# Optimization experiments

Hardware: AMD Instinct MI355X
Metric: run time of the kernel (lower is better)

Reference implementation:

```python
import jax, jax.numpy as jnp
import numpy as np

B, S, H = 4, 2048, 576
NH, NKV, HD = 9, 3, 64
GROUPS = NH // NKV
ROPE_THETA = 100000.0
MAX_POS = 8192


def _rope_tables():
    inv_freq = 1.0 / (ROPE_THETA ** (jnp.arange(0, HD, 2, dtype=jnp.float32) / HD))
    t = jnp.arange(MAX_POS, dtype=jnp.float32)
    freqs = jnp.outer(t, inv_freq)              # [MAX_POS, HD//2]
    emb = jnp.concatenate([freqs, freqs], axis=-1)  # [MAX_POS, HD]
    return jnp.cos(emb), jnp.sin(emb)


def _rotate_half(x):
    x1, x2 = x[..., : HD // 2], x[..., HD // 2 :]
    return jnp.concatenate([-x2, x1], axis=-1)


def setup_inputs() -> dict:
    key = jax.random.key(0)
    k1, k2, k3, k4, k5 = jax.random.split(key, 5)
    hidden_states = jax.random.normal(k1, (B, S, H), dtype=jnp.float32)
    # causal additive mask [B,1,S,S]: 0 where allowed, large negative above diagonal
    causal = jnp.triu(jnp.ones((S, S), dtype=bool), k=1)
    attention_mask = jnp.where(causal, jnp.float32(-1e9), jnp.float32(0.0))[None, None]
    attention_mask = jnp.broadcast_to(attention_mask, (B, 1, S, S))
    position_ids = jnp.broadcast_to(jnp.arange(S, dtype=jnp.int32)[None, :], (B, S))
    scale = 1.0 / np.sqrt(H)
    Wq = jax.random.normal(k2, (NH * HD, H), dtype=jnp.float32) * scale
    Wk = jax.random.normal(k3, (NKV * HD, H), dtype=jnp.float32) * scale
    Wv = jax.random.normal(k4, (NKV * HD, H), dtype=jnp.float32) * scale
    Wo = jax.random.normal(k5, (H, NH * HD), dtype=jnp.float32) * scale
    return {"hidden_states": hidden_states, "attention_mask": attention_mask,
            "position_ids": position_ids, "Wq": Wq, "Wk": Wk, "Wv": Wv, "Wo": Wo}


def reference(hidden_states, attention_mask, position_ids, Wq, Wk, Wv, Wo):
    bsz, q_len, _ = hidden_states.shape
    cos_cached, sin_cached = _rope_tables()
    # projections (nn.Linear: x @ W.T), reshape to [B, heads, S, HD]
    q = (hidden_states @ Wq.T).reshape(bsz, q_len, NH, HD).transpose(0, 2, 1, 3)
    k = (hidden_states @ Wk.T).reshape(bsz, q_len, NKV, HD).transpose(0, 2, 1, 3)
    v = (hidden_states @ Wv.T).reshape(bsz, q_len, NKV, HD).transpose(0, 2, 1, 3)
    # RoPE: gather cos/sin per position, broadcast over heads
    cos = cos_cached[position_ids][:, None]  # [B,1,S,HD]
    sin = sin_cached[position_ids][:, None]
    q = q * cos + _rotate_half(q) * sin
    k = k * cos + _rotate_half(k) * sin
    # GQA: repeat_interleave kv heads
    k = jnp.repeat(k, GROUPS, axis=1)  # [B,NH,S,HD]
    v = jnp.repeat(v, GROUPS, axis=1)
    scores = jnp.einsum('bhqd,bhkd->bhqk', q, k) / np.sqrt(HD)
    scores = scores + attention_mask
    probs = jax.nn.softmax(scores.astype(jnp.float32), axis=-1).astype(q.dtype)
    attn = jnp.einsum('bhqk,bhkd->bhqd', probs, v)
    attn = attn.transpose(0, 2, 1, 3).reshape(bsz, q_len, NH * HD)
    return attn @ Wo.T
```

## Files before the change

### kernel.cpp

```cpp
#include <hip/hip_runtime.h>
#include <hip/hip_bf16.h>
#include <math.h>

#define Bsz 4
#define Slen 2048
#define Hdim 576
#define NH 9
#define NKV 3
#define HD 64

typedef __bf16 bf16_t;
typedef __bf16 bf16x8 __attribute__((ext_vector_type(8)));
typedef float f32x4 __attribute__((ext_vector_type(4)));
typedef float f32x16 __attribute__((ext_vector_type(16)));
typedef unsigned int u32;
typedef unsigned int u32x4 __attribute__((ext_vector_type(4)));

static __device__ __forceinline__ bf16x8 load_cvt8(const float* __restrict__ src){
  float4 f0 = *reinterpret_cast<const float4*>(src);
  float4 f1 = *reinterpret_cast<const float4*>(src + 4);
  bf16x8 v;
  v[0]=(bf16_t)f0.x; v[1]=(bf16_t)f0.y; v[2]=(bf16_t)f0.z; v[3]=(bf16_t)f0.w;
  v[4]=(bf16_t)f1.x; v[5]=(bf16_t)f1.y; v[6]=(bf16_t)f1.z; v[7]=(bf16_t)f1.w;
  return v;
}

static __device__ __forceinline__ void gload16(const bf16_t* g, bf16_t* l){
  __builtin_amdgcn_global_load_lds((const __attribute__((address_space(1))) void*)g,
                                   (__attribute__((address_space(3))) void*)l, 16, 0, 0);
}

__global__ void rope_table_kernel(float* __restrict__ cost, float* __restrict__ sint){
  int i = blockIdx.x * blockDim.x + threadIdx.x;
  if (i >= Slen * 32) return;
  int j = i & 31;
  int p = i >> 5;
  double invf = pow(100000.0, -(double)j / 32.0);
  double ang = (double)p * invf;
  cost[i] = (float)cos(ang);
  sint[i] = (float)sin(ang);
}

__global__ void precast_kernel(const float* __restrict__ X,
                               const float* __restrict__ Wq,
                               const float* __restrict__ Wk,
                               const float* __restrict__ Wv,
                               const float* __restrict__ Wo,
                               bf16_t* __restrict__ Xb,
                               bf16_t* __restrict__ Wb,
                               bf16_t* __restrict__ Wob)
{
  const int NX  = 8192 * 576 / 8;
  const int NWq = 576 * 576 / 8;
  const int NWk = 192 * 576 / 8;
  const int NWo = 576 * 576 / 8;
  int i = blockIdx.x * blockDim.x + threadIdx.x;
  const int total = NX + NWq + 2 * NWk + NWo;
  if (i >= total) return;
  const float* src; bf16_t* dst; int off;
  if (i < NX)                    { src = X;  dst = Xb;            off = i; }
  else if (i < NX + NWq)         { src = Wq; dst = Wb;            off = i - NX; }
  else if (i < NX + NWq + NWk)   { src = Wk; dst = Wb + 331776;   off = i - NX - NWq; }
  else if (i < NX + NWq + 2*NWk) { src = Wv; dst = Wb + 442368;   off = i - NX - NWq - NWk; }
  else                           { src = Wo; dst = Wob;           off = i - NX - NWq - 2*NWk; }
  *reinterpret_cast<bf16x8*>(dst + (size_t)off * 8) = load_cvt8(src + (size_t)off * 8);
}

__launch_bounds__(256)
__global__ void qkv_gemm_kernel(const bf16_t* __restrict__ Xb,
                                const bf16_t* __restrict__ Wb,
                                bf16_t* __restrict__ qbuf,
                                bf16_t* __restrict__ kbuf,
                                bf16_t* __restrict__ vtbuf)
{
  __shared__ bf16_t Ald[2][128 * 64];
  __shared__ bf16_t Bld[2][64 * 64];
  const int t = threadIdx.x, l = t & 63, w = t >> 6;
  const int wm = w >> 1, wn = w & 1;
  const int lane16 = l & 15, grp = l >> 4;
  const int m0 = blockIdx.x * 128;
  const int nt = blockIdx.y;
  const int nrow0 = nt * 64;

  const int sr = l >> 3;
  const int sc = ((l & 7) ^ sr) * 8;

  f32x4 acc[4][2];
  #pragma unroll
  for (int mi = 0; mi < 4; ++mi)
    #pragma unroll
    for (int ni = 0; ni < 2; ++ni)
      acc[mi][ni] = (f32x4){0.f, 0.f, 0.f, 0.f};

  auto STAGE = [&](int kt, int buf){
    const int k0 = kt * 64;
    #pragma unroll
    for (int u = 0; u < 4; ++u)
      gload16(Xb + (size_t)(m0 + w * 32 + u * 8 + sr) * Hdim + k0 + sc,
              &Ald[buf][(w * 32 + u * 8) * 64]);
    #pragma unroll
    for (int u = 0; u < 2; ++u)
      gload16(Wb + (size_t)(nrow0 + w * 16 + u * 8 + sr) * Hdim + k0 + sc,
              &Bld[buf][(w * 16 + u * 8) * 64]);
  };

  STAGE(0, 0);
  asm volatile("s_waitcnt vmcnt(0)" ::: "memory");
  __syncthreads();

  const int sl7 = lane16 & 7;
  for (int kt = 0; kt < 9; ++kt){
    const int buf = kt & 1;
    if (kt + 1 < 9) STAGE(kt + 1, buf ^ 1);
    #pragma unroll
    for (int ks = 0; ks < 2; ++ks){
      bf16x8 a[4], bb[2];
      #pragma unroll
      for (int mi = 0; mi < 4; ++mi){
        int row = wm * 64 + mi * 16 + lane16;
        a[mi] = *reinterpret_cast<const bf16x8*>(&Ald[buf][row * 64 + (((ks * 4 + grp) ^ sl7) * 8)]);
      }
      #pragma unroll
      for (int ni = 0; ni < 2; ++ni){
        int row = wn * 32 + ni * 16 + lane16;
        bb[ni] = *reinterpret_cast<const bf16x8*>(&Bld[buf][row * 64 + (((ks * 4 + grp) ^ sl7) * 8)]);
      }
      #pragma unroll
      for (int mi = 0; mi < 4; ++mi)
        #pragma unroll
        for (int ni = 0; ni < 2; ++ni)
          acc[mi][ni] = __builtin_amdgcn_mfma_f32_16x16x32_bf16(a[mi], bb[ni], acc[mi][ni], 0, 0, 0);
    }
    if (kt + 1 < 9){
      asm volatile("s_waitcnt vmcnt(0)" ::: "memory");
      __syncthreads();
    }
  }

  #pragma unroll
  for (int mi = 0; mi < 4; ++mi){
    #pragma unroll
    for (int ni = 0; ni < 2; ++ni){
      #pragma unroll
      for (int j = 0; j < 4; ++j){
        int m = m0 + wm * 64 + mi * 16 + grp * 4 + j;
        int dl = wn * 32 + ni * 16 + lane16;
        int b = m >> 11;
        int s = m & 2047;
        bf16_t v = (bf16_t)acc[mi][ni][j];
        if (nt < 9)
          qbuf[(((size_t)b * NH + nt) * Slen + s) * HD + dl] = v;
        else if (nt < 12)
          kbuf[(((size_t)b * NKV + (nt - 9)) * Slen + s) * HD + dl] = v;
        else
          vtbuf[(((size_t)b * NKV + (nt - 12)) * HD + dl) * Slen + s] = v;
      }
    }
  }
}

__global__ void rope_apply_all(bf16_t* __restrict__ qkbuf, const int* __restrict__ pos_ids,
                               const float* __restrict__ cost, const float* __restrict__ sint,
                               float qscale)
{
  int idx = blockIdx.x * blockDim.x + threadIdx.x;
  const int qrows = Bsz * NH * Slen;
  const int total = qrows + Bsz * NKV * Slen;
  if (idx >= total) return;
  const bool isq = idx < qrows;
  int s = idx & (Slen - 1);
  int b = isq ? idx / (NH * Slen) : (idx - qrows) / (NKV * Slen);
  float scale = isq ? qscale : 1.0f;
  bf16_t* row = qkbuf + (size_t)idx * HD;
  int pos = pos_ids[b * Slen + s];
  const float* cp = cost + (size_t)pos * 32;
  const float* sp = sint + (size_t)pos * 32;
  float x[64];
  #pragma unroll
  for (int v = 0; v < 8; ++v){
    bf16x8 t8 = *reinterpret_cast<const bf16x8*>(row + v * 8);
    #pragma unroll
    for (int i = 0; i < 8; ++i) x[v * 8 + i] = (float)t8[i];
  }
  bf16_t o[64];
  #pragma unroll
  for (int j = 0; j < 32; ++j){
    float c = cp[j], sn = sp[j];
    o[j]      = (bf16_t)((x[j] * c - x[j + 32] * sn) * scale);
    o[j + 32] = (bf16_t)((x[j + 32] * c + x[j] * sn) * scale);
  }
  #pragma unroll
  for (int v = 0; v < 8; ++v)
    *reinterpret_cast<bf16x8*>(row + v * 8) = *reinterpret_cast<bf16x8*>(o + v * 8);
}

__launch_bounds__(128)
__global__ void flash_attn_kernel(const bf16_t* __restrict__ qbuf,
                                  const bf16_t* __restrict__ kbuf,
                                  const bf16_t* __restrict__ vtbuf,
                                  bf16_t* __restrict__ attn_out)
{
  __shared__ bf16_t Kld[2][64 * 64];
  __shared__ bf16_t Vld[2][64 * 64];
  const int t = threadIdx.x, l = t & 63, w = t >> 6;
  const int l32 = l & 31, hi = l >> 5;

  const int flat = blockIdx.x;
  const int iq = flat / 36;
  const int bh = flat % 36;
  const int qt = (iq & 1) ? (iq >> 1) : (31 - (iq >> 1));
  const int b = bh / NH, h = bh % NH, kvh = h / (NH / NKV);

  const bf16_t* qp = qbuf + ((size_t)b * NH + h) * Slen * HD;
  const bf16_t* kp = kbuf + ((size_t)b * NKV + kvh) * Slen * HD;
  const bf16_t* vp = vtbuf + ((size_t)b * NKV + kvh) * HD * Slen;

  const int q0 = qt * 64 + w * 32;
  bf16x8 aq[4];
  #pragma unroll
  for (int ds = 0; ds < 4; ++ds)
    aq[ds] = *reinterpret_cast<const bf16x8*>(qp + (size_t)(q0 + l32) * HD + ds * 16 + hi * 8);

  f32x16 acco[2];
  #pragma unroll
  for (int db = 0; db < 2; ++db)
    #pragma unroll
    for (int r = 0; r < 16; ++r) acco[db][r] = 0.f;
  float mrun = -1e30f, lrun = 0.f;

  const int sr = l >> 3;
  const int sc = ((l & 7) ^ sr) * 8;

  const int ntiles = qt + 1;
  int cur = 0;

  {
    #pragma unroll
    for (int u = 0; u < 4; ++u){
      int r = (w * 4 + u) * 8 + sr;
      gload16(kp + (size_t)r * HD + sc, &Kld[0][(w * 4 + u) * 512]);
      gload16(vp + (size_t)r * Slen + sc, &Vld[0][(w * 4 + u) * 512]);
    }
  }
  asm volatile("s_waitcnt vmcnt(0)" ::: "memory");
  __syncthreads();

  for (int kb = 0; kb < ntiles; ++kb){
    if (kb + 1 < ntiles){
      const int k0_ = (kb + 1) * 64;
      #pragma unroll
      for (int u = 0; u < 4; ++u){
        int r = (w * 4 + u) * 8 + sr;
        gload16(kp + (size_t)(k0_ + r) * HD + sc, &Kld[cur ^ 1][(w * 4 + u) * 512]);
        gload16(vp + (size_t)r * Slen + k0_ + sc, &Vld[cur ^ 1][(w * 4 + u) * 512]);
      }
    }

    f32x16 sacc[2];
    #pragma unroll
    for (int kb2 = 0; kb2 < 2; ++kb2)
      #pragma unroll
      for (int r = 0; r < 16; ++r) sacc[kb2][r] = 0.f;

    __builtin_amdgcn_s_setprio(1);
    #pragma unroll
    for (int ds = 0; ds < 4; ++ds){
      #pragma unroll
      for (int kb2 = 0; kb2 < 2; ++kb2){
        int row = kb2 * 32 + l32;
        bf16x8 ak = *reinterpret_cast<const bf16x8*>(
            &Kld[cur][row * 64 + (((ds * 2 + hi) ^ (row & 7)) * 8)]);
        sacc[kb2] = __builtin_amdgcn_mfma_f32_32x32x16_bf16(ak, aq[ds], sacc[kb2], 0, 0, 0);
      }
    }
    __builtin_amdgcn_s_setprio(0);

    if (kb == qt){
      const int q_wt = w * 32 + l32;
      #pragma unroll
      for (int kb2 = 0; kb2 < 2; ++kb2)
        #pragma unroll
        for (int r = 0; r < 16; ++r){
          int k_wt = kb2 * 32 + (r & 3) + 8 * (r >> 2) + 4 * hi;
          if (k_wt > q_wt) sacc[kb2][r] = -1e30f;
        }
    }

    float tmax;
    {
      float m0_ = fmaxf(sacc[0][0], sacc[0][1]);
      #pragma unroll
      for (int r = 2; r < 16; ++r) m0_ = fmaxf(m0_, sacc[0][r]);
      float m1_ = fmaxf(sacc[1][0], sacc[1][1]);
      #pragma unroll
      for (int r = 2; r < 16; ++r) m1_ = fmaxf(m1_, sacc[1][r]);
      tmax = fmaxf(m0_, m1_);
    }
    tmax = fmaxf(tmax, __shfl_xor(tmax, 32, 64));

    if (__ballot(tmax - mrun > 8.f)){
      float mnew = fmaxf(mrun, tmax);
      float sf = __builtin_amdgcn_exp2f(mrun - mnew);
      lrun *= sf;
      #pragma unroll
      for (int db = 0; db < 2; ++db)
        #pragma unroll
        for (int r = 0; r < 16; ++r) acco[db][r] *= sf;
      mrun = mnew;
    }

    float rs0 = 0.f, rs1 = 0.f;
    #pragma unroll
    for (int kb2 = 0; kb2 < 2; ++kb2){
      #pragma unroll
      for (int r = 0; r < 16; ++r){
        float p = __builtin_amdgcn_exp2f(sacc[kb2][r] - mrun);
        sacc[kb2][r] = p;
        if (kb2) rs1 += p; else rs0 += p;
      }
    }
    float rsum = rs0 + rs1;
    rsum += __shfl_xor(rsum, 32, 64);
    lrun += rsum;

    u32x4 pa[4];
    #pragma unroll
    for (int kb2 = 0; kb2 < 2; ++kb2){
      u32 wv[8];
      #pragma unroll
      for (int j = 0; j < 8; ++j){
        float lo = sacc[kb2][2 * j], hp = sacc[kb2][2 * j + 1];
        asm("v_cvt_pk_bf16_f32 %0, %1, %2" : "=v"(wv[j]) : "v"(lo), "v"(hp));
      }
      asm volatile("v_permlane32_swap_b32 %0, %1" : "+v"(wv[0]), "+v"(wv[2]));
      asm volatile("v_permlane32_swap_b32 %0, %1" : "+v"(wv[1]), "+v"(wv[3]));
      asm volatile("v_permlane32_swap_b32 %0, %1" : "+v"(wv[4]), "+v"(wv[6]));
      asm volatile("v_permlane32_swap_b32 %0, %1" : "+v"(wv[5]), "+v"(wv[7]));
      pa[2 * kb2]     = (u32x4){wv[0], wv[1], wv[2], wv[3]};
      pa[2 * kb2 + 1] = (u32x4){wv[4], wv[5], wv[6], wv[7]};
    }

    __builtin_amdgcn_s_setprio(1);
    #pragma unroll
    for (int ks = 0; ks < 4; ++ks){
      #pragma unroll
      for (int db = 0; db < 2; ++db){
        int row = db * 32 + l32;
        bf16x8 av = *reinterpret_cast<const bf16x8*>(
            &Vld[cur][row * 64 + (((ks * 2 + hi) ^ (row & 7)) * 8)]);
        acco[db] = __builtin_amdgcn_mfma_f32_32x32x16_bf16(
            av, __builtin_bit_cast(bf16x8, pa[ks]), acco[db], 0, 0, 0);
      }
    }
    __builtin_amdgcn_s_setprio(0);

    asm volatile("s_waitcnt vmcnt(0)" ::: "memory");
    __syncthreads();
    cur ^= 1;
  }

  const float linv = 1.0f / lrun;
  const int srow = q0 + l32;
  bf16_t* orow = attn_out + ((size_t)b * Slen + srow) * (NH * HD) + h * HD;
  #pragma unroll
  for (int db = 0; db < 2; ++db){
    #pragma unroll
    for (int j = 0; j < 8; ++j){
      int r = 2 * j;
      int d = db * 32 + (r & 3) + 8 * (r >> 2) + 4 * hi;
      u32 pw;
      float lo = acco[db][r] * linv, hp = acco[db][r + 1] * linv;
      asm("v_cvt_pk_bf16_f32 %0, %1, %2" : "=v"(pw) : "v"(lo), "v"(hp));
      *reinterpret_cast<u32*>(orow + d) = pw;
    }
  }
}

__launch_bounds__(256)
__global__ void out_gemm_kernel(const bf16_t* __restrict__ A,
                                const bf16_t* __restrict__ Wob,
                                float* __restrict__ out)
{
  __shared__ bf16_t Ald[2][128 * 64];
  __shared__ bf16_t Bld[2][64 * 64];
  const int t = threadIdx.x, l = t & 63, w = t >> 6;
  const int wm = w >> 1, wn = w & 1;
  const int lane16 = l & 15, grp = l >> 4;
  const int m0 = blockIdx.x * 128;
  const int nt = blockIdx.y;
  const int nrow0 = nt * 64;

  const int sr = l >> 3;
  const int sc = ((l & 7) ^ sr) * 8;

  f32x4 acc[4][2];
  #pragma unroll
  for (int mi = 0; mi < 4; ++mi)
    #pragma unroll
    for (int ni = 0; ni < 2; ++ni)
      acc[mi][ni] = (f32x4){0.f, 0.f, 0.f, 0.f};

  auto STAGE = [&](int kt, int buf){
    const int k0 = kt * 64;
    #pragma unroll
    for (int u = 0; u < 4; ++u)
      gload16(A + (size_t)(m0 + w * 32 + u * 8 + sr) * Hdim + k0 + sc,
              &Ald[buf][(w * 32 + u * 8) * 64]);
    #pragma unroll
    for (int u = 0; u < 2; ++u)
      gload16(Wob + (size_t)(nrow0 + w * 16 + u * 8 + sr) * Hdim + k0 + sc,
              &Bld[buf][(w * 16 + u * 8) * 64]);
  };

  STAGE(0, 0);
  asm volatile("s_waitcnt vmcnt(0)" ::: "memory");
  __syncthreads();

  const int sl7 = lane16 & 7;
  for (int kt = 0; kt < 9; ++kt){
    const int buf = kt & 1;
    if (kt + 1 < 9) STAGE(kt + 1, buf ^ 1);
    #pragma unroll
    for (int ks = 0; ks < 2; ++ks){
      bf16x8 a[4], bb[2];
      #pragma unroll
      for (int mi = 0; mi < 4; ++mi){
        int row = wm * 64 + mi * 16 + lane16;
        a[mi] = *reinterpret_cast<const bf16x8*>(&Ald[buf][row * 64 + (((ks * 4 + grp) ^ sl7) * 8)]);
      }
      #pragma unroll
      for (int ni = 0; ni < 2; ++ni){
        int row = wn * 32 + ni * 16 + lane16;
        bb[ni] = *reinterpret_cast<const bf16x8*>(&Bld[buf][row * 64 + (((ks * 4 + grp) ^ sl7) * 8)]);
      }
      #pragma unroll
      for (int mi = 0; mi < 4; ++mi)
        #pragma unroll
        for (int ni = 0; ni < 2; ++ni)
          acc[mi][ni] = __builtin_amdgcn_mfma_f32_16x16x32_bf16(a[mi], bb[ni], acc[mi][ni], 0, 0, 0);
    }
    if (kt + 1 < 9){
      asm volatile("s_waitcnt vmcnt(0)" ::: "memory");
      __syncthreads();
    }
  }

  #pragma unroll
  for (int mi = 0; mi < 4; ++mi){
    #pragma unroll
    for (int ni = 0; ni < 2; ++ni){
      #pragma unroll
      for (int j = 0; j < 4; ++j){
        int m = m0 + wm * 64 + mi * 16 + grp * 4 + j;
        int n = nrow0 + wn * 32 + ni * 16 + lane16;
        out[(size_t)m * Hdim + n] = acc[mi][ni][j];
      }
    }
  }
}

extern "C" void kernel_launch(void* const* d_in, const int* in_sizes, int n_in,
                              void* d_out, int out_size, void* d_ws, size_t ws_size,
                              hipStream_t stream) {
  const float* X   = (const float*)d_in[0];
  const int* pos   = (const int*)d_in[2];
  const float* Wq  = (const float*)d_in[3];
  const float* Wk  = (const float*)d_in[4];
  const float* Wv  = (const float*)d_in[5];
  const float* Wo  = (const float*)d_in[6];
  float* out = (float*)d_out;

  char* ws = (char*)d_ws;
  float* cost = (float*)ws;
  float* sint = (float*)(ws + 262144);
  bf16_t* qb  = (bf16_t*)(ws + 524288);
  bf16_t* kb  = qb + (size_t)Bsz * NH * Slen * HD;
  bf16_t* vt  = kb + (size_t)Bsz * NKV * Slen * HD;
  bf16_t* Xb  = vt + (size_t)Bsz * NKV * Slen * HD;
  bf16_t* ab  = Xb;
  bf16_t* Wb  = Xb + (size_t)8192 * 576;
  bf16_t* Wob = Wb + (size_t)960 * 576;

  const float QSCALE = 0.125f * 1.44269504088896f;

  rope_table_kernel<<<dim3((Slen * 32 + 255) / 256), dim3(256), 0, stream>>>(cost, sint);
  precast_kernel<<<dim3(2736), dim3(256), 0, stream>>>(X, Wq, Wk, Wv, Wo, Xb, Wb, Wob);
  qkv_gemm_kernel<<<dim3(64, 15), dim3(256), 0, stream>>>(Xb, Wb, qb, kb, vt);
  rope_apply_all<<<dim3((Bsz * (NH + NKV) * Slen + 255) / 256), dim3(256), 0, stream>>>(qb, pos, cost, sint, QSCALE);
  flash_attn_kernel<<<dim3(1152), dim3(128), 0, stream>>>(qb, kb, vt, ab);
  out_gemm_kernel<<<dim3(64, 9), dim3(256), 0, stream>>>(ab, Wob, out);
}
```

Measured before the change: 119.6 us.

## Split long causal query tiles across two KV segments with combine kernel

Query tiles 16-31 now have their KV range split in two: tiles 0-15 and tiles 16 up to the diagonal. Each half is handled by a separate block that writes unnormalized bf16 partial outputs plus running max and sum to workspace. A new combine kernel merges the two halves with log-sum-exp rescaling. The aim is to balance the causal workload across 1728 equal-sized blocks, removing the long-tail blocks that gate the kernel's end. The cost is an extra launch, extra global traffic for the partials, and bf16 rounding of the partials before they are merged.

```diff
diff --git a/kernel.cpp b/kernel.cpp
--- a/kernel.cpp
+++ b/kernel.cpp
@@ -53,9 +53,8 @@
   const int NX  = 8192 * 576 / 8;
   const int NWq = 576 * 576 / 8;
   const int NWk = 192 * 576 / 8;
-  const int NWo = 576 * 576 / 8;
   int i = blockIdx.x * blockDim.x + threadIdx.x;
-  const int total = NX + NWq + 2 * NWk + NWo;
+  const int total = NX + NWq + 2 * NWk + NWq;
   if (i >= total) return;
   const float* src; bf16_t* dst; int off;
   if (i < NX)                    { src = X;  dst = Xb;            off = i; }
@@ -198,7 +197,9 @@
 __global__ void flash_attn_kernel(const bf16_t* __restrict__ qbuf,
                                   const bf16_t* __restrict__ kbuf,
                                   const bf16_t* __restrict__ vtbuf,
-                                  bf16_t* __restrict__ attn_out)
+                                  bf16_t* __restrict__ attn_out,
+                                  u32* __restrict__ part_O,
+                                  float* __restrict__ part_ml)
 {
   __shared__ bf16_t Kld[2][64 * 64];
   __shared__ bf16_t Vld[2][64 * 64];
@@ -206,9 +207,15 @@
   const int l32 = l & 31, hi = l >> 5;
 
   const int flat = blockIdx.x;
-  const int iq = flat / 36;
+  const int v = flat / 36;
   const int bh = flat % 36;
-  const int qt = (iq & 1) ? (iq >> 1) : (31 - (iq >> 1));
+  int qt, t0, t1, seg;
+  if (v < 16){ qt = 16 + v; t0 = 0; t1 = 16; seg = 0; }
+  else {
+    int i = (v - 16) >> 1;
+    if (((v - 16) & 1) == 0){ qt = 15 - i; t0 = 0; t1 = qt + 1; seg = -1; }
+    else                    { qt = 31 - i; t0 = 16; t1 = qt + 1; seg = 1; }
+  }
   const int b = bh / NH, h = bh % NH, kvh = h / (NH / NKV);
 
   const bf16_t* qp = qbuf + ((size_t)b * NH + h) * Slen * HD;
@@ -231,30 +238,23 @@
   const int sr = l >> 3;
   const int sc = ((l & 7) ^ sr) * 8;
 
-  const int ntiles = qt + 1;
-  int cur = 0;
-
-  {
+  auto STAGE = [&](int kt, int buf){
+    const int k0 = kt * 64;
     #pragma unroll
     for (int u = 0; u < 4; ++u){
       int r = (w * 4 + u) * 8 + sr;
-      gload16(kp + (size_t)r * HD + sc, &Kld[0][(w * 4 + u) * 512]);
-      gload16(vp + (size_t)r * Slen + sc, &Vld[0][(w * 4 + u) * 512]);
-    }
-  }
+      gload16(kp + (size_t)(k0 + r) * HD + sc, &Kld[buf][(w * 4 + u) * 512]);
+      gload16(vp + (size_t)r * Slen + k0 + sc, &Vld[buf][(w * 4 + u) * 512]);
+    }
+  };
+
+  int cur = 0;
+  STAGE(t0, 0);
   asm volatile("s_waitcnt vmcnt(0)" ::: "memory");
   __syncthreads();
 
-  for (int kb = 0; kb < ntiles; ++kb){
-    if (kb + 1 < ntiles){
-      const int k0_ = (kb + 1) * 64;
-      #pragma unroll
-      for (int u = 0; u < 4; ++u){
-        int r = (w * 4 + u) * 8 + sr;
-        gload16(kp + (size_t)(k0_ + r) * HD + sc, &Kld[cur ^ 1][(w * 4 + u) * 512]);
-        gload16(vp + (size_t)r * Slen + k0_ + sc, &Vld[cur ^ 1][(w * 4 + u) * 512]);
-      }
-    }
+  for (int kb = t0; kb < t1; ++kb){
+    if (kb + 1 < t1) STAGE(kb + 1, cur ^ 1);
 
     f32x16 sacc[2];
     #pragma unroll
@@ -359,20 +359,81 @@
     cur ^= 1;
   }
 
-  const float linv = 1.0f / lrun;
-  const int srow = q0 + l32;
-  bf16_t* orow = attn_out + ((size_t)b * Slen + srow) * (NH * HD) + h * HD;
-  #pragma unroll
-  for (int db = 0; db < 2; ++db){
-    #pragma unroll
-    for (int j = 0; j < 8; ++j){
-      int r = 2 * j;
-      int d = db * 32 + (r & 3) + 8 * (r >> 2) + 4 * hi;
-      u32 pw;
-      float lo = acco[db][r] * linv, hp = acco[db][r + 1] * linv;
-      asm("v_cvt_pk_bf16_f32 %0, %1, %2" : "=v"(pw) : "v"(lo), "v"(hp));
-      *reinterpret_cast<u32*>(orow + d) = pw;
-    }
+  if (seg < 0){
+    const float linv = 1.0f / lrun;
+    const int srow = q0 + l32;
+    bf16_t* orow = attn_out + ((size_t)b * Slen + srow) * (NH * HD) + h * HD;
+    #pragma unroll
+    for (int db = 0; db < 2; ++db){
+      #pragma unroll
+      for (int j = 0; j < 8; ++j){
+        int r = 2 * j;
+        int d = db * 32 + (r & 3) + 8 * (r >> 2) + 4 * hi;
+        u32 pw;
+        float lo = acco[db][r] * linv, hp = acco[db][r + 1] * linv;
+        asm("v_cvt_pk_bf16_f32 %0, %1, %2" : "=v"(pw) : "v"(lo), "v"(hp));
+        *reinterpret_cast<u32*>(orow + d) = pw;
+      }
+    }
+  } else {
+    const int slot = (bh * 16 + (qt - 16)) * 2 + seg;
+    u32* po = part_O + ((size_t)slot * 2 + w) * 1024;
+    float* pml = part_ml + ((size_t)slot * 2 + w) * 64;
+    #pragma unroll
+    for (int db = 0; db < 2; ++db){
+      #pragma unroll
+      for (int j = 0; j < 8; ++j){
+        int r = 2 * j;
+        int d = db * 32 + (r & 3) + 8 * (r >> 2) + 4 * hi;
+        u32 pw;
+        float lo = acco[db][r], hp = acco[db][r + 1];
+        asm("v_cvt_pk_bf16_f32 %0, %1, %2" : "=v"(pw) : "v"(lo), "v"(hp));
+        po[(d >> 1) * 32 + l32] = pw;
+      }
+    }
+    if (hi == 0){ pml[l32] = mrun; pml[32 + l32] = lrun; }
+  }
+}
+
+__launch_bounds__(128)
+__global__ void combine_kernel(const u32* __restrict__ part_O,
+                               const float* __restrict__ part_ml,
+                               bf16_t* __restrict__ attn_out)
+{
+  const int idx = blockIdx.x;
+  const int bh = idx % 36, qtm = idx / 36;
+  const int qt = 16 + qtm;
+  const int b = bh / NH, h = bh % NH;
+  const int t = threadIdx.x;
+  const int q = t & 31, wg = (t >> 5) & 1, half = t >> 6;
+  const int slot0 = (bh * 16 + qtm) * 2;
+
+  const float* pml0 = part_ml + ((size_t)(slot0 + 0) * 2 + wg) * 64;
+  const float* pml1 = part_ml + ((size_t)(slot0 + 1) * 2 + wg) * 64;
+  float m1 = pml0[q], l1 = pml0[32 + q];
+  float m2 = pml1[q], l2 = pml1[32 + q];
+  float m = fmaxf(m1, m2);
+  float a1 = __builtin_amdgcn_exp2f(m1 - m);
+  float a2 = __builtin_amdgcn_exp2f(m2 - m);
+  float linv = 1.0f / (l1 * a1 + l2 * a2);
+  a1 *= linv; a2 *= linv;
+
+  const u32* po0 = part_O + ((size_t)(slot0 + 0) * 2 + wg) * 1024;
+  const u32* po1 = part_O + ((size_t)(slot0 + 1) * 2 + wg) * 1024;
+  const int s = qt * 64 + wg * 32 + q;
+  bf16_t* orow = attn_out + ((size_t)b * Slen + s) * (NH * HD) + h * HD;
+
+  #pragma unroll
+  for (int u = 0; u < 16; ++u){
+    int dp = half * 16 + u;
+    u32 v1 = po0[dp * 32 + q], v2 = po1[dp * 32 + q];
+    float lo = a1 * __builtin_bit_cast(float, v1 << 16)
+             + a2 * __builtin_bit_cast(float, v2 << 16);
+    float hv = a1 * __builtin_bit_cast(float, v1 & 0xffff0000u)
+             + a2 * __builtin_bit_cast(float, v2 & 0xffff0000u);
+    u32 pw;
+    asm("v_cvt_pk_bf16_f32 %0, %1, %2" : "=v"(pw) : "v"(lo), "v"(hv));
+    *reinterpret_cast<u32*>(orow + 2 * dp) = pw;
   }
 }
 
@@ -480,6 +541,8 @@
   bf16_t* ab  = Xb;
   bf16_t* Wb  = Xb + (size_t)8192 * 576;
   bf16_t* Wob = Wb + (size_t)960 * 576;
+  u32*  part_O  = (u32*)(Wob + (size_t)576 * 576);
+  float* part_ml = (float*)(part_O + (size_t)1152 * 2 * 1024);
 
   const float QSCALE = 0.125f * 1.44269504088896f;
 
@@ -487,6 +550,7 @@
   precast_kernel<<<dim3(2736), dim3(256), 0, stream>>>(X, Wq, Wk, Wv, Wo, Xb, Wb, Wob);
   qkv_gemm_kernel<<<dim3(64, 15), dim3(256), 0, stream>>>(Xb, Wb, qb, kb, vt);
   rope_apply_all<<<dim3((Bsz * (NH + NKV) * Slen + 255) / 256), dim3(256), 0, stream>>>(qb, pos, cost, sint, QSCALE);
-  flash_attn_kernel<<<dim3(1152), dim3(128), 0, stream>>>(qb, kb, vt, ab);
+  flash_attn_kernel<<<dim3(1728), dim3(128), 0, stream>>>(qb, kb, vt, ab, part_O, part_ml);
+  combine_kernel<<<dim3(576), dim3(128), 0, stream>>>(part_O, part_ml, ab);
   out_gemm_kernel<<<dim3(64, 9), dim3(256), 0, stream>>>(ab, Wob, out);
 }
```

Measured after the change: 119.4 us. No clear change (-0.2%).
